# Performance work log

Hardware: AMD Instinct MI355X
Metric: run time of the kernel (lower is better)

Reference implementation:

```python
import jax, jax.numpy as jnp
import numpy as np

N_NODES = 100000
N_EDGES = 1200000
N_GRAPHS = 128
D_IN = 64
D_HID = 64
N_CLASSES = 10


def gcn_conv(x, row, col, W, b):
    """PyG GCNConv: h = x@W; add self-loops; sym-norm deg^-1/2 gather-scatter; + bias."""
    n = x.shape[0]
    h = x @ W  # [N, out]
    loop = jnp.arange(n)
    r = jnp.concatenate([row, loop])
    c = jnp.concatenate([col, loop])
    deg = jax.ops.segment_sum(jnp.ones_like(c, dtype=x.dtype), c, num_segments=n)
    dinv = jax.lax.rsqrt(jnp.maximum(deg, 1.0))  # with self-loops deg >= 1
    norm = dinv[r] * dinv[c]  # [E+N]
    msg = h[r] * norm[:, None]  # gather + per-edge scale
    out = jax.ops.segment_sum(msg, c, num_segments=n)  # scatter-add at targets
    return out + b


def global_mean_pool(x, batch, num_graphs):
    s = jax.ops.segment_sum(x, batch, num_segments=num_graphs)
    cnt = jax.ops.segment_sum(jnp.ones((x.shape[0],), dtype=x.dtype), batch, num_segments=num_graphs)
    return s / jnp.maximum(cnt, 1.0)[:, None]


def setup_inputs() -> dict:
    key = jax.random.key(0)
    ks = jax.random.split(key, 12)
    x = jax.random.normal(ks[0], (N_NODES, D_IN), dtype=jnp.float32)
    edge_index = jax.random.randint(ks[1], (2, N_EDGES), 0, N_NODES, dtype=jnp.int64)
    batch = jnp.sort(jax.random.randint(ks[2], (N_NODES,), 0, N_GRAPHS, dtype=jnp.int64))

    def glorot(k, fan_in, fan_out):
        lim = (6.0 / (fan_in + fan_out)) ** 0.5
        return jax.random.uniform(k, (fan_in, fan_out), jnp.float32, -lim, lim)

    return {
        "x": x,
        "edge_index": edge_index,
        "batch": batch,
        "W1": glorot(ks[3], D_IN, D_HID),
        "b1": jnp.zeros((D_HID,), jnp.float32),
        "W2": glorot(ks[4], D_HID, D_HID),
        "b2": jnp.zeros((D_HID,), jnp.float32),
        "W3": glorot(ks[5], D_HID, D_HID),
        "b3": jnp.zeros((D_HID,), jnp.float32),
        "linW": glorot(ks[6], D_HID, N_CLASSES),
        "linb": jnp.zeros((N_CLASSES,), jnp.float32),
    }


def reference(x, edge_index, batch, W1, b1, W2, b2, W3, b3, linW, linb):
    row, col = edge_index[0], edge_index[1]
    h = jax.nn.relu(gcn_conv(x, row, col, W1, b1))
    h = jax.nn.relu(gcn_conv(h, row, col, W2, b2))
    h = gcn_conv(h, row, col, W3, b3)
    g = global_mean_pool(h, batch, N_GRAPHS)  # [B, hidden]
    # dropout p=0.5 is identity in eval mode (training=False)
    return g @ linW + linb  # [B, num_classes]
```

## Files before the change

### kernel.cpp

```cpp
#include <hip/hip_runtime.h>
#include <hip/hip_bf16.h>


#define N_NODES 100000
#define N_EDGES 1200000
#define N_GRAPHS 128
#define D 64
#define N_CLASSES 10

#define NB 512
#define BSZ 196
#define PEB 4096
#define PEB4 (PEB/4)

typedef unsigned short ushort_t;

__device__ __forceinline__ float bf2f(ushort_t u) {
    union { unsigned int i; float f; } v;
    v.i = ((unsigned int)u) << 16;
    return v.f;
}

__global__ void init_k(int* __restrict__ bcount,
                       float* __restrict__ gsum, float* __restrict__ cnt) {
    int i = blockIdx.x * 256 + threadIdx.x;
    if (i < NB) bcount[i] = 0;
    if (i < N_GRAPHS * D) gsum[i] = 0.0f;
    if (i < N_GRAPHS) cnt[i] = 0.0f;
}

__global__ void count_k(const int4* __restrict__ col4, int* __restrict__ bcount, int E4) {
    __shared__ int h[NB];
    for (int i = threadIdx.x; i < NB; i += 256) h[i] = 0;
    __syncthreads();
    int base = blockIdx.x * PEB4;
#pragma unroll
    for (int k = 0; k < 4; ++k) {
        int idx = base + k * 256 + threadIdx.x;
        if (idx < E4) {
            int4 c = col4[idx];
            atomicAdd(&h[c.x / BSZ], 1);
            atomicAdd(&h[c.y / BSZ], 1);
            atomicAdd(&h[c.z / BSZ], 1);
            atomicAdd(&h[c.w / BSZ], 1);
        }
    }
    __syncthreads();
    for (int i = threadIdx.x; i < NB; i += 256)
        if (h[i]) atomicAdd(&bcount[i], h[i]);
}

__global__ void scan_k(const int* __restrict__ bcount, int* __restrict__ bstart,
                       int* __restrict__ bcursor) {
    __shared__ int s[NB];
    int t = threadIdx.x;
    int v0 = bcount[t];
    s[t] = v0;
    __syncthreads();
    for (int off = 1; off < NB; off <<= 1) {
        int v = (t >= off) ? s[t - off] : 0;
        __syncthreads();
        s[t] += v;
        __syncthreads();
    }
    int ex = s[t] - v0;
    bstart[t] = ex;
    bcursor[t] = ex;
}

__global__ void scatter_k(const int4* __restrict__ row4, const int4* __restrict__ col4,
                          int* __restrict__ bcursor, int2* __restrict__ part, int E4) {
    __shared__ int h[NB], gb[NB], c2[NB];
    for (int i = threadIdx.x; i < NB; i += 256) { h[i] = 0; c2[i] = 0; }
    __syncthreads();
    int base = blockIdx.x * PEB4;
    int4 rr[4], cc[4];
    bool ok[4];
#pragma unroll
    for (int k = 0; k < 4; ++k) {
        int idx = base + k * 256 + threadIdx.x;
        ok[k] = idx < E4;
        if (ok[k]) {
            rr[k] = row4[idx];
            cc[k] = col4[idx];
            atomicAdd(&h[cc[k].x / BSZ], 1);
            atomicAdd(&h[cc[k].y / BSZ], 1);
            atomicAdd(&h[cc[k].z / BSZ], 1);
            atomicAdd(&h[cc[k].w / BSZ], 1);
        }
    }
    __syncthreads();
    for (int i = threadIdx.x; i < NB; i += 256)
        if (h[i]) gb[i] = atomicAdd(&bcursor[i], h[i]);
    __syncthreads();
#pragma unroll
    for (int k = 0; k < 4; ++k) {
        if (ok[k]) {
            int r[4] = { rr[k].x, rr[k].y, rr[k].z, rr[k].w };
            int c[4] = { cc[k].x, cc[k].y, cc[k].z, cc[k].w };
#pragma unroll
            for (int j = 0; j < 4; ++j) {
                int b = c[j] / BSZ;
                int rk = atomicAdd(&c2[b], 1);
                part[gb[b] + rk] = make_int2(r[j], c[j]);
            }
        }
    }
}

__global__ void sortbuild_k(const int2* __restrict__ part, const int* __restrict__ bstart,
                            const int* __restrict__ bcount, int* __restrict__ csr,
                            int* __restrict__ deg, int* __restrict__ cursor,
                            float* __restrict__ dinv) {
    __shared__ int h[256], st[256], c2[256];
    int b = blockIdx.x, t = threadIdx.x;
    int ebeg = bstart[b];
    int cntE = bcount[b];
    h[t] = 0; c2[t] = 0;
    __syncthreads();
    for (int e = ebeg + t; e < ebeg + cntE; e += 256) {
        int2 rc = part[e];
        atomicAdd(&h[rc.y - b * BSZ], 1);
    }
    __syncthreads();
    int hv = h[t];
    for (int off = 1; off < 256; off <<= 1) {
        int v = (t >= off) ? h[t - off] : 0;
        __syncthreads();
        h[t] += v;
        __syncthreads();
    }
    st[t] = h[t] - hv;
    __syncthreads();
    int node = b * BSZ + t;
    if (t < BSZ && node < N_NODES) {
        deg[node] = hv;
        dinv[node] = rsqrtf((float)(hv + 1));
        cursor[node] = ebeg + st[t] + hv;
    }
    for (int e = ebeg + t; e < ebeg + cntE; e += 256) {
        int2 rc = part[e];
        int cl = rc.y - b * BSZ;
        int rk = atomicAdd(&c2[cl], 1);
        csr[ebeg + st[cl] + rk] = rc.x;
    }
}

__global__ __launch_bounds__(256) void gemm_k(
        const float* __restrict__ X, const float* __restrict__ W,
        const float* __restrict__ dinv, ushort_t* __restrict__ H, int n, int relu_in) {
    __shared__ float Xs[4][D];
    int tid = threadIdx.x, wave = tid >> 6, lane = tid & 63;
    float wcol[D];
#pragma unroll
    for (int k = 0; k < D; ++k) wcol[k] = W[k * D + lane];
    for (int row0 = blockIdx.x * 4; row0 < n; row0 += gridDim.x * 4) {
        int row = row0 + wave;
        if (row < n) {
            float xv = X[row * D + lane];
            if (relu_in) xv = fmaxf(xv, 0.0f);
            Xs[wave][lane] = xv;
            float acc = 0.0f;
#pragma unroll
            for (int k = 0; k < D; ++k) acc += Xs[wave][k] * wcol[k];
            __hip_bfloat16 hb = __float2bfloat16(acc * dinv[row]);
            H[(size_t)row * D + lane] = *(ushort_t*)&hb;
        }
    }
}

__global__ void gather_k(const ushort_t* __restrict__ Hp, const int* __restrict__ csr,
                         const int* __restrict__ cursor, const int* __restrict__ deg,
                         const float* __restrict__ dinv, const float* __restrict__ b,
                         float* __restrict__ O, int n) {
    int c = blockIdx.x * 4 + (threadIdx.x >> 6);
    if (c >= n) return;
    int lane = threadIdx.x & 63;
    int end = cursor[c];
    int dg = deg[c];
    float acc = bf2f(Hp[(size_t)c * D + lane]);
    for (int j = end - dg; j < end; j += 64) {
        int idx = j + lane;
        int s = (idx < end) ? csr[idx] : 0;
        int cnt = min(64, end - j);
        int k = 0;
        for (; k + 4 <= cnt; k += 4) {
            int r0 = __shfl(s, k);
            int r1 = __shfl(s, k + 1);
            int r2 = __shfl(s, k + 2);
            int r3 = __shfl(s, k + 3);
            float v0 = bf2f(Hp[(size_t)r0 * D + lane]);
            float v1 = bf2f(Hp[(size_t)r1 * D + lane]);
            float v2 = bf2f(Hp[(size_t)r2 * D + lane]);
            float v3 = bf2f(Hp[(size_t)r3 * D + lane]);
            acc += v0 + v1 + v2 + v3;
        }
        for (; k < cnt; ++k) {
            int r0 = __shfl(s, k);
            acc += bf2f(Hp[(size_t)r0 * D + lane]);
        }
    }
    O[(size_t)c * D + lane] = b[lane] + dinv[c] * acc;
}

#define POOL_CHUNK 64
__global__ void pool_k(const float* __restrict__ H, const int* __restrict__ batch,
                       float* __restrict__ gsum, float* __restrict__ cnt, int n) {
    int wid = blockIdx.x * 4 + (threadIdx.x >> 6);
    int lane = threadIdx.x & 63;
    int start = wid * POOL_CHUNK;
    if (start >= n) return;
    int m = min(POOL_CHUNK, n - start);
    int bv = batch[min(start + lane, n - 1)];
    int cur = __shfl(bv, 0);
    float acc = 0.0f;
    int run = 0;
    for (int k = 0; k < m; ++k) {
        int bb = __shfl(bv, k);
        if (bb != cur) {
            atomicAdd(&gsum[cur * D + lane], acc);
            if (lane == 0) atomicAdd(&cnt[cur], (float)run);
            cur = bb; acc = 0.0f; run = 0;
        }
        acc += H[(size_t)(start + k) * D + lane];
        ++run;
    }
    atomicAdd(&gsum[cur * D + lane], acc);
    if (lane == 0) atomicAdd(&cnt[cur], (float)run);
}

__global__ void final_k(const float* __restrict__ gsum, const float* __restrict__ cnt,
                        const float* __restrict__ linW, const float* __restrict__ linb,
                        float* __restrict__ out) {
    int tid = blockIdx.x * 256 + threadIdx.x;
    if (tid >= N_GRAPHS * N_CLASSES) return;
    int b = tid / N_CLASSES, c = tid % N_CLASSES;
    float inv = 1.0f / fmaxf(cnt[b], 1.0f);
    float acc = linb[c];
#pragma unroll
    for (int k = 0; k < D; ++k)
        acc += gsum[b * D + k] * inv * linW[k * N_CLASSES + c];
    out[tid] = acc;
}

extern "C" void kernel_launch(void* const* d_in, const int* in_sizes, int n_in,
                              void* d_out, int out_size, void* d_ws, size_t ws_size,
                              hipStream_t stream) {
    const float* x    = (const float*)d_in[0];
    const int*   ei   = (const int*)  d_in[1];
    const int*   batch= (const int*)  d_in[2];
    const float* W1   = (const float*)d_in[3];
    const float* b1   = (const float*)d_in[4];
    const float* W2   = (const float*)d_in[5];
    const float* b2   = (const float*)d_in[6];
    const float* W3   = (const float*)d_in[7];
    const float* b3   = (const float*)d_in[8];
    const float* linW = (const float*)d_in[9];
    const float* linb = (const float*)d_in[10];
    float* out = (float*)d_out;

    const int N = N_NODES, E = N_EDGES, E4 = N_EDGES / 4;
    const int4* row4 = (const int4*)ei;
    const int4* col4 = (const int4*)(ei + E);

    int* wsi = (int*)d_ws;
    float* dinv   = (float*)wsi;
    int*   deg    = wsi + 100352;
    int*   cursor = deg + 100352;
    int*   csr    = cursor + 100352;
    int*   bcount = csr + 1200128;
    int*   bstart = bcount + 512;
    int*   bcursor= bstart + 512;
    int2*  part   = (int2*)(bcursor + 512);
    ushort_t* bufH = (ushort_t*)(part + 1200128);
    float* bufA   = (float*)(bufH + (size_t)N * D);
    float* gsum   = bufA + (size_t)N * D;
    float* cnt    = gsum + N_GRAPHS * D;

    const int nb_part  = (E + PEB - 1) / PEB;
    const int nb_gather= (N + 3) / 4;
    const int nb_gemm  = 2048;
    const int nwaves   = (N + POOL_CHUNK - 1) / POOL_CHUNK;
    const int nb_pool  = (nwaves + 3) / 4;

    init_k<<<(N_GRAPHS * D + 255) / 256, 256, 0, stream>>>(bcount, gsum, cnt);
    count_k<<<nb_part, 256, 0, stream>>>(col4, bcount, E4);
    scan_k<<<1, NB, 0, stream>>>(bcount, bstart, bcursor);
    scatter_k<<<nb_part, 256, 0, stream>>>(row4, col4, bcursor, part, E4);
    sortbuild_k<<<NB, 256, 0, stream>>>(part, bstart, bcount, csr, deg, cursor, dinv);

    gemm_k<<<nb_gemm, 256, 0, stream>>>(x, W1, dinv, bufH, N, 0);
    gather_k<<<nb_gather, 256, 0, stream>>>(bufH, csr, cursor, deg, dinv, b1, bufA, N);
    gemm_k<<<nb_gemm, 256, 0, stream>>>(bufA, W2, dinv, bufH, N, 1);
    gather_k<<<nb_gather, 256, 0, stream>>>(bufH, csr, cursor, deg, dinv, b2, bufA, N);
    gemm_k<<<nb_gemm, 256, 0, stream>>>(bufA, W3, dinv, bufH, N, 1);
    gather_k<<<nb_gather, 256, 0, stream>>>(bufH, csr, cursor, deg, dinv, b3, bufA, N);

    pool_k<<<nb_pool, 256, 0, stream>>>(bufA, batch, gsum, cnt, N);
    final_k<<<(N_GRAPHS * N_CLASSES + 255) / 256, 256, 0, stream>>>(gsum, cnt, linW, linb, out);
}
```

Measured before the change: 362.2 us.

## Pack edge partitions, store intermediates in bf16, fuse pooling into final gather

Edge partition entries are packed into one int (source<<8 | local target) instead of an int2, which halves partition traffic. Intermediate layer activations are stored as bf16 instead of fp32, so the gather writes and the next GEMM reads carry half the bytes. The last gather now atomically adds each node's output straight into the per-graph sums, which removes the separate pool kernel and the final activation write. Graph node counts move into count_k. The cost is extra bf16 rounding of activations and 100k per-lane global atomics onto only 128 graph rows, which may contend.

```diff
diff --git a/kernel.cpp b/kernel.cpp
--- a/kernel.cpp
+++ b/kernel.cpp
@@ -19,6 +19,10 @@
     union { unsigned int i; float f; } v;
     v.i = ((unsigned int)u) << 16;
     return v.f;
+}
+__device__ __forceinline__ ushort_t f2bf(float f) {
+    __hip_bfloat16 hb = __float2bfloat16(f);
+    return *(ushort_t*)&hb;
 }
 
 __global__ void init_k(int* __restrict__ bcount,
@@ -29,9 +33,13 @@
     if (i < N_GRAPHS) cnt[i] = 0.0f;
 }
 
-__global__ void count_k(const int4* __restrict__ col4, int* __restrict__ bcount, int E4) {
+__global__ void count_k(const int4* __restrict__ col4, int* __restrict__ bcount,
+                        const int* __restrict__ batch, float* __restrict__ cnt,
+                        int E4, int n) {
     __shared__ int h[NB];
+    __shared__ int bh[N_GRAPHS];
     for (int i = threadIdx.x; i < NB; i += 256) h[i] = 0;
+    if (threadIdx.x < N_GRAPHS) bh[threadIdx.x] = 0;
     __syncthreads();
     int base = blockIdx.x * PEB4;
 #pragma unroll
@@ -45,9 +53,13 @@
             atomicAdd(&h[c.w / BSZ], 1);
         }
     }
+    for (int i = blockIdx.x * 256 + threadIdx.x; i < n; i += gridDim.x * 256)
+        atomicAdd(&bh[batch[i]], 1);
     __syncthreads();
     for (int i = threadIdx.x; i < NB; i += 256)
         if (h[i]) atomicAdd(&bcount[i], h[i]);
+    if (threadIdx.x < N_GRAPHS && bh[threadIdx.x])
+        atomicAdd(&cnt[threadIdx.x], (float)bh[threadIdx.x]);
 }
 
 __global__ void scan_k(const int* __restrict__ bcount, int* __restrict__ bstart,
@@ -69,7 +81,7 @@
 }
 
 __global__ void scatter_k(const int4* __restrict__ row4, const int4* __restrict__ col4,
-                          int* __restrict__ bcursor, int2* __restrict__ part, int E4) {
+                          int* __restrict__ bcursor, int* __restrict__ part, int E4) {
     __shared__ int h[NB], gb[NB], c2[NB];
     for (int i = threadIdx.x; i < NB; i += 256) { h[i] = 0; c2[i] = 0; }
     __syncthreads();
@@ -100,15 +112,16 @@
             int c[4] = { cc[k].x, cc[k].y, cc[k].z, cc[k].w };
 #pragma unroll
             for (int j = 0; j < 4; ++j) {
-                int b = c[j] / BSZ;
-                int rk = atomicAdd(&c2[b], 1);
-                part[gb[b] + rk] = make_int2(r[j], c[j]);
+                int bk = c[j] / BSZ;
+                int dl = c[j] - bk * BSZ;
+                int rk = atomicAdd(&c2[bk], 1);
+                part[gb[bk] + rk] = (r[j] << 8) | dl;
             }
         }
     }
 }
 
-__global__ void sortbuild_k(const int2* __restrict__ part, const int* __restrict__ bstart,
+__global__ void sortbuild_k(const int* __restrict__ part, const int* __restrict__ bstart,
                             const int* __restrict__ bcount, int* __restrict__ csr,
                             int* __restrict__ deg, int* __restrict__ cursor,
                             float* __restrict__ dinv) {
@@ -118,10 +131,8 @@
     int cntE = bcount[b];
     h[t] = 0; c2[t] = 0;
     __syncthreads();
-    for (int e = ebeg + t; e < ebeg + cntE; e += 256) {
-        int2 rc = part[e];
-        atomicAdd(&h[rc.y - b * BSZ], 1);
-    }
+    for (int e = ebeg + t; e < ebeg + cntE; e += 256)
+        atomicAdd(&h[part[e] & 255], 1);
     __syncthreads();
     int hv = h[t];
     for (int off = 1; off < 256; off <<= 1) {
@@ -139,16 +150,16 @@
         cursor[node] = ebeg + st[t] + hv;
     }
     for (int e = ebeg + t; e < ebeg + cntE; e += 256) {
-        int2 rc = part[e];
-        int cl = rc.y - b * BSZ;
+        int p = part[e];
+        int cl = p & 255;
         int rk = atomicAdd(&c2[cl], 1);
-        csr[ebeg + st[cl] + rk] = rc.x;
-    }
-}
-
-__global__ __launch_bounds__(256) void gemm_k(
+        csr[ebeg + st[cl] + rk] = p >> 8;
+    }
+}
+
+__global__ __launch_bounds__(256) void gemm_f32_k(
         const float* __restrict__ X, const float* __restrict__ W,
-        const float* __restrict__ dinv, ushort_t* __restrict__ H, int n, int relu_in) {
+        const float* __restrict__ dinv, ushort_t* __restrict__ H, int n) {
     __shared__ float Xs[4][D];
     int tid = threadIdx.x, wave = tid >> 6, lane = tid & 63;
     float wcol[D];
@@ -157,14 +168,31 @@
     for (int row0 = blockIdx.x * 4; row0 < n; row0 += gridDim.x * 4) {
         int row = row0 + wave;
         if (row < n) {
-            float xv = X[row * D + lane];
-            if (relu_in) xv = fmaxf(xv, 0.0f);
-            Xs[wave][lane] = xv;
+            Xs[wave][lane] = X[(size_t)row * D + lane];
             float acc = 0.0f;
 #pragma unroll
             for (int k = 0; k < D; ++k) acc += Xs[wave][k] * wcol[k];
-            __hip_bfloat16 hb = __float2bfloat16(acc * dinv[row]);
-            H[(size_t)row * D + lane] = *(ushort_t*)&hb;
+            H[(size_t)row * D + lane] = f2bf(acc * dinv[row]);
+        }
+    }
+}
+
+__global__ __launch_bounds__(256) void gemm_bf16_k(
+        const ushort_t* __restrict__ U, const float* __restrict__ W,
+        const float* __restrict__ dinv, ushort_t* __restrict__ H, int n) {
+    __shared__ float Xs[4][D];
+    int tid = threadIdx.x, wave = tid >> 6, lane = tid & 63;
+    float wcol[D];
+#pragma unroll
+    for (int k = 0; k < D; ++k) wcol[k] = W[k * D + lane];
+    for (int row0 = blockIdx.x * 4; row0 < n; row0 += gridDim.x * 4) {
+        int row = row0 + wave;
+        if (row < n) {
+            Xs[wave][lane] = fmaxf(bf2f(U[(size_t)row * D + lane]), 0.0f);
+            float acc = 0.0f;
+#pragma unroll
+            for (int k = 0; k < D; ++k) acc += Xs[wave][k] * wcol[k];
+            H[(size_t)row * D + lane] = f2bf(acc * dinv[row]);
         }
     }
 }
@@ -172,7 +200,7 @@
 __global__ void gather_k(const ushort_t* __restrict__ Hp, const int* __restrict__ csr,
                          const int* __restrict__ cursor, const int* __restrict__ deg,
                          const float* __restrict__ dinv, const float* __restrict__ b,
-                         float* __restrict__ O, int n) {
+                         ushort_t* __restrict__ O, int n) {
     int c = blockIdx.x * 4 + (threadIdx.x >> 6);
     if (c >= n) return;
     int lane = threadIdx.x & 63;
@@ -200,33 +228,43 @@
             acc += bf2f(Hp[(size_t)r0 * D + lane]);
         }
     }
-    O[(size_t)c * D + lane] = b[lane] + dinv[c] * acc;
-}
-
-#define POOL_CHUNK 64
-__global__ void pool_k(const float* __restrict__ H, const int* __restrict__ batch,
-                       float* __restrict__ gsum, float* __restrict__ cnt, int n) {
-    int wid = blockIdx.x * 4 + (threadIdx.x >> 6);
+    O[(size_t)c * D + lane] = f2bf(b[lane] + dinv[c] * acc);
+}
+
+__global__ void gather_pool_k(const ushort_t* __restrict__ Hp, const int* __restrict__ csr,
+                              const int* __restrict__ cursor, const int* __restrict__ deg,
+                              const float* __restrict__ dinv, const float* __restrict__ b,
+                              const int* __restrict__ batch, float* __restrict__ gsum,
+                              int n) {
+    int c = blockIdx.x * 4 + (threadIdx.x >> 6);
+    if (c >= n) return;
     int lane = threadIdx.x & 63;
-    int start = wid * POOL_CHUNK;
-    if (start >= n) return;
-    int m = min(POOL_CHUNK, n - start);
-    int bv = batch[min(start + lane, n - 1)];
-    int cur = __shfl(bv, 0);
-    float acc = 0.0f;
-    int run = 0;
-    for (int k = 0; k < m; ++k) {
-        int bb = __shfl(bv, k);
-        if (bb != cur) {
-            atomicAdd(&gsum[cur * D + lane], acc);
-            if (lane == 0) atomicAdd(&cnt[cur], (float)run);
-            cur = bb; acc = 0.0f; run = 0;
-        }
-        acc += H[(size_t)(start + k) * D + lane];
-        ++run;
-    }
-    atomicAdd(&gsum[cur * D + lane], acc);
-    if (lane == 0) atomicAdd(&cnt[cur], (float)run);
+    int end = cursor[c];
+    int dg = deg[c];
+    float acc = bf2f(Hp[(size_t)c * D + lane]);
+    for (int j = end - dg; j < end; j += 64) {
+        int idx = j + lane;
+        int s = (idx < end) ? csr[idx] : 0;
+        int cnt = min(64, end - j);
+        int k = 0;
+        for (; k + 4 <= cnt; k += 4) {
+            int r0 = __shfl(s, k);
+            int r1 = __shfl(s, k + 1);
+            int r2 = __shfl(s, k + 2);
+            int r3 = __shfl(s, k + 3);
+            float v0 = bf2f(Hp[(size_t)r0 * D + lane]);
+            float v1 = bf2f(Hp[(size_t)r1 * D + lane]);
+            float v2 = bf2f(Hp[(size_t)r2 * D + lane]);
+            float v3 = bf2f(Hp[(size_t)r3 * D + lane]);
+            acc += v0 + v1 + v2 + v3;
+        }
+        for (; k < cnt; ++k) {
+            int r0 = __shfl(s, k);
+            acc += bf2f(Hp[(size_t)r0 * D + lane]);
+        }
+    }
+    float val = b[lane] + dinv[c] * acc;
+    atomicAdd(&gsum[batch[c] * D + lane], val);
 }
 
 __global__ void final_k(const float* __restrict__ gsum, const float* __restrict__ cnt,
@@ -268,34 +306,32 @@
     int*   deg    = wsi + 100352;
     int*   cursor = deg + 100352;
     int*   csr    = cursor + 100352;
-    int*   bcount = csr + 1200128;
+    int*   part   = csr + 1200128;
+    int*   bcount = part + 1200128;
     int*   bstart = bcount + 512;
     int*   bcursor= bstart + 512;
-    int2*  part   = (int2*)(bcursor + 512);
-    ushort_t* bufH = (ushort_t*)(part + 1200128);
-    float* bufA   = (float*)(bufH + (size_t)N * D);
-    float* gsum   = bufA + (size_t)N * D;
+    ushort_t* bufH = (ushort_t*)(bcursor + 512);
+    ushort_t* bufA = bufH + (size_t)N * D;
+    float* gsum   = (float*)(bufA + (size_t)N * D);
     float* cnt    = gsum + N_GRAPHS * D;
 
     const int nb_part  = (E + PEB - 1) / PEB;
     const int nb_gather= (N + 3) / 4;
     const int nb_gemm  = 2048;
-    const int nwaves   = (N + POOL_CHUNK - 1) / POOL_CHUNK;
-    const int nb_pool  = (nwaves + 3) / 4;
 
     init_k<<<(N_GRAPHS * D + 255) / 256, 256, 0, stream>>>(bcount, gsum, cnt);
-    count_k<<<nb_part, 256, 0, stream>>>(col4, bcount, E4);
+    count_k<<<nb_part, 256, 0, stream>>>(col4, bcount, batch, cnt, E4, N);
     scan_k<<<1, NB, 0, stream>>>(bcount, bstart, bcursor);
     scatter_k<<<nb_part, 256, 0, stream>>>(row4, col4, bcursor, part, E4);
     sortbuild_k<<<NB, 256, 0, stream>>>(part, bstart, bcount, csr, deg, cursor, dinv);
 
-    gemm_k<<<nb_gemm, 256, 0, stream>>>(x, W1, dinv, bufH, N, 0);
+    gemm_f32_k<<<nb_gemm, 256, 0, stream>>>(x, W1, dinv, bufH, N);
     gather_k<<<nb_gather, 256, 0, stream>>>(bufH, csr, cursor, deg, dinv, b1, bufA, N);
-    gemm_k<<<nb_gemm, 256, 0, stream>>>(bufA, W2, dinv, bufH, N, 1);
+    gemm_bf16_k<<<nb_gemm, 256, 0, stream>>>(bufA, W2, dinv, bufH, N);
     gather_k<<<nb_gather, 256, 0, stream>>>(bufH, csr, cursor, deg, dinv, b2, bufA, N);
-    gemm_k<<<nb_gemm, 256, 0, stream>>>(bufA, W3, dinv, bufH, N, 1);
-    gather_k<<<nb_gather, 256, 0, stream>>>(bufH, csr, cursor, deg, dinv, b3, bufA, N);
-
-    pool_k<<<nb_pool, 256, 0, stream>>>(bufA, batch, gsum, cnt, N);
+    gemm_bf16_k<<<nb_gemm, 256, 0, stream>>>(bufA, W3, dinv, bufH, N);
+    gather_pool_k<<<nb_gather, 256, 0, stream>>>(bufH, csr, cursor, deg, dinv, b3,
+                                                 batch, gsum, N);
+
     final_k<<<(N_GRAPHS * N_CLASSES + 255) / 256, 256, 0, stream>>>(gsum, cnt, linW, linb, out);
 }
```

Result: slower. 397.6 us (+9.8%).
